# Performance work log

Measured on AMD Instinct MI355X. Metric: run time of the kernel, lower is better.

Reference implementation:

```python
import jax, jax.numpy as jnp
import numpy as np

N = 100_000      # nodes
E = 1_600_000    # edges (avg degree 16)
IN = 512         # in_feats
HID = 4          # hidden_feats (forced equal to num_heads=4 by the mean(h,2) in forward)
H1 = 4           # heads in layer 1
OUT = 128        # out_feats
NEG_SLOPE = 0.2  # DGL GATConv leaky_relu default


def setup_inputs() -> dict:
    key = jax.random.key(0)
    ks = jax.random.split(key, 12)
    nfeats = jax.random.normal(ks[0], (N, IN), jnp.float32)
    efeats = jax.random.normal(ks[1], (E, 8), jnp.float32)  # unused by the module
    src = jax.random.randint(ks[2], (E,), 0, N, dtype=jnp.int32)
    dst = jax.random.randint(ks[3], (E,), 0, N, dtype=jnp.int32)
    # layer 1 params (in=IN, heads=H1, per-head out=HID)
    fc1_w = jax.random.normal(ks[4], (IN, H1 * HID), jnp.float32) / np.sqrt(IN)
    attn_l1 = jax.random.normal(ks[5], (H1, HID), jnp.float32) / np.sqrt(HID)
    attn_r1 = jax.random.normal(ks[6], (H1, HID), jnp.float32) / np.sqrt(HID)
    bias1 = jnp.zeros((H1 * HID,), jnp.float32)
    # layer 2 params (in=H1=4 after mean over feature dim, heads=1, out=OUT)
    fc2_w = jax.random.normal(ks[7], (HID, 1 * OUT), jnp.float32) / np.sqrt(HID)
    attn_l2 = jax.random.normal(ks[8], (1, OUT), jnp.float32) / np.sqrt(OUT)
    attn_r2 = jax.random.normal(ks[9], (1, OUT), jnp.float32) / np.sqrt(OUT)
    bias2 = jnp.zeros((OUT,), jnp.float32)
    return {"nfeats": nfeats, "efeats": efeats, "src": src, "dst": dst,
            "fc1_w": fc1_w, "attn_l1": attn_l1, "attn_r1": attn_r1, "bias1": bias1,
            "fc2_w": fc2_w, "attn_l2": attn_l2, "attn_r2": attn_r2, "bias2": bias2}


def gat_layer(x, src, dst, fc_w, attn_l, attn_r, bias, heads, d_out):
    # projection: (N, in) -> (N, H, D)
    h = (x @ fc_w).reshape(-1, heads, d_out)
    el = jnp.einsum('nhd,hd->nh', h, attn_l)   # (N, H)
    er = jnp.einsum('nhd,hd->nh', h, attn_r)
    e = jax.nn.leaky_relu(el[src] + er[dst], NEG_SLOPE)  # (E, H)
    # segment softmax over incoming edges of each dst node
    m = jax.lax.stop_gradient(jax.ops.segment_max(e, dst, num_segments=N))
    ex = jnp.exp(e - m[dst])
    denom = jax.ops.segment_sum(ex, dst, num_segments=N)
    alpha = ex / denom[dst]                    # (E, H)
    msg = alpha[:, :, None] * h[src]           # (E, H, D)
    rst = jax.ops.segment_sum(msg, dst, num_segments=N)  # (N, H, D)
    return rst + bias.reshape(1, heads, d_out)


def reference(nfeats, efeats, src, dst, fc1_w, attn_l1, attn_r1, bias1,
              fc2_w, attn_l2, attn_r2, bias2):
    h = gat_layer(nfeats, src, dst, fc1_w, attn_l1, attn_r1, bias1, H1, HID)  # (N,4,4)
    h = jnp.mean(h, axis=2)        # faithful to th.mean(h, 2): mean over per-head feat dim -> (N,4)
    h = jax.nn.relu(h)
    h = gat_layer(h, src, dst, fc2_w, attn_l2, attn_r2, bias2, 1, OUT)        # (N,1,OUT)
    return h.reshape(N, OUT)       # flatten(1)
```

## Files before the change

kernel.cpp:

```cpp
#include <hip/hip_runtime.h>
#include <math.h>

#define IN_F 512
#define OUTF 128
#define NEG_SLOPE 0.2f

#define P1T 256
#define TK 16
#define PITCH 20

#define NPB 128
#define NBMAX 784
#define EPB 4096
#define SRCMASK 0x1FFFF
#define CAP 2944

#define WSH_BYTES (IN_F * 12 * 4)
#define XS_BYTES  (P1T * PITCH * 4)
#define SMEM_A    (WSH_BYTES + XS_BYTES)

__global__ void k_prep(const float* __restrict__ fc1, const float* __restrict__ al1,
                       const float* __restrict__ ar1, const float* __restrict__ fc2,
                       const float* __restrict__ al2, const float* __restrict__ ar2,
                       float* __restrict__ wfold, float* __restrict__ w2al,
                       float* __restrict__ w2ar, int* __restrict__ bucketCursor) {
  int t = threadIdx.x;
  if (blockIdx.x == 0) {
    int k = t;
#pragma unroll
    for (int h = 0; h < 4; ++h) {
      float wl = 0.f, wr = 0.f, wb = 0.f;
#pragma unroll
      for (int j = 0; j < 4; ++j) {
        float wv = fc1[k * 16 + h * 4 + j];
        wl = fmaf(wv, al1[h * 4 + j], wl);
        wr = fmaf(wv, ar1[h * 4 + j], wr);
        wb += wv;
      }
      wfold[k * 12 + h] = wl;
      wfold[k * 12 + 4 + h] = wr;
      wfold[k * 12 + 8 + h] = 0.25f * wb;
    }
  } else {
    if (t < 8) {
      int h = t >> 1;
      const float* a = (t & 1) ? ar2 : al2;
      float s = 0.f;
#pragma unroll 16
      for (int c = 0; c < OUTF; ++c) s += fc2[h * OUTF + c] * a[c];
      if (t & 1) w2ar[h] = s; else w2al[h] = s;
    }
    for (int i = t; i < NBMAX; i += 512) bucketCursor[i] = 0;
  }
}

__global__ __launch_bounds__(P1T) void k_A(
    const float* __restrict__ x, const float* __restrict__ wf,
    float* __restrict__ pk1, float* __restrict__ er1, int n,
    const int* __restrict__ src, const int* __restrict__ dst,
    int* __restrict__ bucketCursor, unsigned* __restrict__ ep, int e,
    int projBlocks)
{
  __shared__ __align__(16) char smem[SMEM_A];
  const int t = threadIdx.x;

  if ((int)blockIdx.x < projBlocks) {
    float* wsh = (float*)smem;
    float* xs  = (float*)(smem + WSH_BYTES);
    const int lane = t & 63;
    const int wv = t >> 6;
    const int rowBase = blockIdx.x * P1T;
    const int wrow = rowBase + wv * 64;
    const int myRow = rowBase + t;

    for (int i = t * 4; i < IN_F * 12; i += P1T * 4)
      *(float4*)&wsh[i] = *(const float4*)&wf[i];
    __syncthreads();

    float acc[12];
#pragma unroll
    for (int c = 0; c < 12; ++c) acc[c] = 0.f;

    float4 st[4];
#pragma unroll
    for (int i = 0; i < 4; ++i) {
      int f4 = lane + i * 64;
      int r = f4 >> 2, c4 = (f4 & 3) << 2;
      int row = wrow + r;
      st[i] = (row < n) ? *(const float4*)&x[(size_t)row * IN_F + c4]
                        : make_float4(0.f, 0.f, 0.f, 0.f);
    }

    for (int tile = 0; tile < IN_F / TK; ++tile) {
#pragma unroll
      for (int i = 0; i < 4; ++i) {
        int f4 = lane + i * 64;
        int r = f4 >> 2, c4 = (f4 & 3) << 2;
        *(float4*)&xs[(wv * 64 + r) * PITCH + c4] = st[i];
      }
      if (tile + 1 < IN_F / TK) {
        int k0 = (tile + 1) * TK;
#pragma unroll
        for (int i = 0; i < 4; ++i) {
          int f4 = lane + i * 64;
          int r = f4 >> 2, c4 = (f4 & 3) << 2;
          int row = wrow + r;
          st[i] = (row < n) ? *(const float4*)&x[(size_t)row * IN_F + k0 + c4]
                            : make_float4(0.f, 0.f, 0.f, 0.f);
        }
      }
      asm volatile("s_waitcnt lgkmcnt(0)" ::: "memory");
      __builtin_amdgcn_sched_barrier(0);
      const int kb = tile * TK;
#pragma unroll
      for (int k4 = 0; k4 < 4; ++k4) {
        float4 xv = *(const float4*)&xs[t * PITCH + k4 * 4];
        float xj[4] = {xv.x, xv.y, xv.z, xv.w};
#pragma unroll
        for (int j = 0; j < 4; ++j) {
          const float* wk = &wsh[(kb + k4 * 4 + j) * 12];
          float4 w0 = *(const float4*)&wk[0];
          float4 w1 = *(const float4*)&wk[4];
          float4 w2 = *(const float4*)&wk[8];
          acc[0]  = fmaf(xj[j], w0.x, acc[0]);   acc[1]  = fmaf(xj[j], w0.y, acc[1]);
          acc[2]  = fmaf(xj[j], w0.z, acc[2]);   acc[3]  = fmaf(xj[j], w0.w, acc[3]);
          acc[4]  = fmaf(xj[j], w1.x, acc[4]);   acc[5]  = fmaf(xj[j], w1.y, acc[5]);
          acc[6]  = fmaf(xj[j], w1.z, acc[6]);   acc[7]  = fmaf(xj[j], w1.w, acc[7]);
          acc[8]  = fmaf(xj[j], w2.x, acc[8]);   acc[9]  = fmaf(xj[j], w2.y, acc[9]);
          acc[10] = fmaf(xj[j], w2.z, acc[10]);  acc[11] = fmaf(xj[j], w2.w, acc[11]);
        }
      }
    }

    if (myRow < n) {
      *(float4*)&pk1[(size_t)myRow * 8 + 0] = make_float4(acc[0], acc[1], acc[2], acc[3]);
      *(float4*)&pk1[(size_t)myRow * 8 + 4] = make_float4(acc[8], acc[9], acc[10], acc[11]);
      *(float4*)&er1[(size_t)myRow * 4] = make_float4(acc[4], acc[5], acc[6], acc[7]);
    }
  } else {
    int* hist = (int*)smem;
    int* base = hist + NBMAX;
    int* lcur = base + NBMAX;
    const int bb = blockIdx.x - projBlocks;
    for (int i = t; i < NBMAX; i += P1T) hist[i] = 0;
    __syncthreads();
    int blockBase = bb * EPB;
#pragma unroll
    for (int i = 0; i < EPB / P1T; ++i) {
      int idx = blockBase + t + i * P1T;
      if (idx < e) atomicAdd(&hist[dst[idx] >> 7], 1);
    }
    __syncthreads();
    for (int i = t; i < NBMAX; i += P1T) {
      if (hist[i] > 0) base[i] = atomicAdd(&bucketCursor[i], hist[i]);
      lcur[i] = 0;
    }
    __syncthreads();
#pragma unroll
    for (int i = 0; i < EPB / P1T; ++i) {
      int idx = blockBase + t + i * P1T;
      if (idx < e) {
        int d = dst[idx];
        int b = d >> 7;
        int off = base[b] + atomicAdd(&lcur[b], 1);
        if (off < CAP)
          ep[(size_t)b * CAP + off] = (unsigned)src[idx] | ((unsigned)(d & (NPB - 1)) << 17);
      }
    }
  }
}

__global__ __launch_bounds__(256) void k_B(
    const unsigned* __restrict__ ep, const int* __restrict__ bucketCursor,
    unsigned* __restrict__ ep2, int* __restrict__ nodeBeg, int* __restrict__ nodeEnd,
    const float* __restrict__ pk1, const float* __restrict__ er1,
    const float* __restrict__ bias1,
    const float* __restrict__ w2al, const float* __restrict__ w2ar,
    float* __restrict__ pk2, float* __restrict__ er2, int n)
{
  __shared__ int cnt[NPB];
  __shared__ int scn[NPB];
  __shared__ int cur[NPB];
  __shared__ unsigned lbuf[CAP];
  int t = threadIdx.x;
  int b = blockIdx.x;
  int nodeBase = b * NPB;
  int m = bucketCursor[b];
  if (m > CAP) m = CAP;
  const unsigned* __restrict__ in = ep + (size_t)b * CAP;
  if (t < NPB) cnt[t] = 0;
  __syncthreads();
  for (int j = t; j < m; j += 256) atomicAdd(&cnt[in[j] >> 17], 1);
  __syncthreads();
  if (t < NPB) scn[t] = cnt[t];
  __syncthreads();
  for (int off = 1; off < NPB; off <<= 1) {
    int v = (t < NPB && t >= off) ? scn[t - off] : 0;
    __syncthreads();
    if (t < NPB) scn[t] += v;
    __syncthreads();
  }
  if (t < NPB) {
    int excl = scn[t] - cnt[t];
    int node = nodeBase + t;
    if (node < n) {
      nodeBeg[node] = b * CAP + excl;
      nodeEnd[node] = b * CAP + excl + cnt[t];
    }
    cur[t] = excl;
  }
  __syncthreads();
  for (int j = t; j < m; j += 256) {
    unsigned p = in[j];
    int pos = atomicAdd(&cur[p >> 17], 1);
    lbuf[pos] = p & SRCMASK;
  }
  __syncthreads();
  for (int i = t; i < m; i += 256) ep2[(size_t)b * CAP + i] = lbuf[i];

#pragma unroll
  for (int half = 0; half < 2; ++half) {
    int w = t + half * 256;
    int i = w >> 2, h = w & 3;
    int node = nodeBase + i;
    bool active = node < n;
    float v = 0.f;
    if (active) {
      int beg = scn[i] - cnt[i], end = scn[i];
      float ern = er1[(size_t)node * 4 + h];
      float den = 0.f, num = 0.f;
      for (int j = beg; j < end; ++j) {
        int s = (int)lbuf[j];
        float el = pk1[(size_t)s * 8 + h];
        float hb = pk1[(size_t)s * 8 + 4 + h];
        float eh = el + ern;
        eh = (eh > 0.f) ? eh : NEG_SLOPE * eh;
        float wg = __expf(eh);
        den += wg;
        num = fmaf(wg, hb, num);
      }
      float mb = 0.25f * (bias1[h*4] + bias1[h*4+1] + bias1[h*4+2] + bias1[h*4+3]);
      v = (end > beg) ? num / den : 0.f;
      v += mb;
      v = (v > 0.f) ? v : 0.f;
    }
    float pl = v * w2al[h];
    float pr = v * w2ar[h];
    pl += __shfl_xor(pl, 1); pl += __shfl_xor(pl, 2);
    pr += __shfl_xor(pr, 1); pr += __shfl_xor(pr, 2);
    if (active) {
      pk2[(size_t)node * 8 + h] = v;
      if (h == 0) { pk2[(size_t)node * 8 + 4] = pl; er2[node] = pr; }
    }
  }
}

__global__ __launch_bounds__(256) void k_bagg2(
    const unsigned* __restrict__ ep2, const int* __restrict__ nodeBeg,
    const int* __restrict__ nodeEnd,
    const float* __restrict__ pk2, const float* __restrict__ er2,
    const float* __restrict__ w2, const float* __restrict__ bias2,
    float* __restrict__ out, int n)
{
  __shared__ float gacc[256 * 4];
  __shared__ float w2s[4 * OUTF];
  __shared__ float b2s[OUTF];
  int t = threadIdx.x;
  int nodeBase = blockIdx.x * 256;
  int nn = nodeBase + t;
  for (int i = t; i < 4 * OUTF; i += 256) w2s[i] = w2[i];
  if (t < OUTF) b2s[t] = bias2[t];
  float g0 = 0.f, g1 = 0.f, g2 = 0.f, g3 = 0.f;
  if (nn < n) {
    int beg = nodeBeg[nn], end = nodeEnd[nn];
    float ern = er2[nn];
    float den = 0.f;
    for (int j = beg; j < end; ++j) {
      int s = (int)ep2[j];
      const float* __restrict__ ps = &pk2[(size_t)s * 8];
      float4 hv = *(const float4*)ps;
      float e = ps[4] + ern;
      e = (e > 0.f) ? e : NEG_SLOPE * e;
      float w = __expf(e);
      den += w;
      g0 = fmaf(w, hv.x, g0); g1 = fmaf(w, hv.y, g1);
      g2 = fmaf(w, hv.z, g2); g3 = fmaf(w, hv.w, g3);
    }
    float inv = (end > beg) ? 1.0f / den : 0.f;
    g0 *= inv; g1 *= inv; g2 *= inv; g3 *= inv;
  }
  gacc[t * 4 + 0] = g0; gacc[t * 4 + 1] = g1;
  gacc[t * 4 + 2] = g2; gacc[t * 4 + 3] = g3;
  __syncthreads();
  for (int idx = t; idx < 256 * (OUTF / 2); idx += 256) {
    int i = idx >> 6;
    int node = nodeBase + i;
    if (node >= n) continue;
    int c = (idx & 63) * 2;
    float gx = gacc[i*4], gy = gacc[i*4+1], gz = gacc[i*4+2], gw = gacc[i*4+3];
    float2 o;
    o.x = gx*w2s[c]   + gy*w2s[OUTF+c]   + gz*w2s[2*OUTF+c]   + gw*w2s[3*OUTF+c]   + b2s[c];
    o.y = gx*w2s[c+1] + gy*w2s[OUTF+c+1] + gz*w2s[2*OUTF+c+1] + gw*w2s[3*OUTF+c+1] + b2s[c+1];
    *(float2*)&out[(size_t)node * OUTF + c] = o;
  }
}

extern "C" void kernel_launch(void* const* d_in, const int* in_sizes, int n_in,
                              void* d_out, int out_size, void* d_ws, size_t ws_size,
                              hipStream_t stream) {
  const float* nfeats = (const float*)d_in[0];
  const int*   srcp   = (const int*)d_in[2];
  const int*   dstp   = (const int*)d_in[3];
  const float* fc1    = (const float*)d_in[4];
  const float* al1    = (const float*)d_in[5];
  const float* ar1    = (const float*)d_in[6];
  const float* bias1  = (const float*)d_in[7];
  const float* fc2    = (const float*)d_in[8];
  const float* al2    = (const float*)d_in[9];
  const float* ar2    = (const float*)d_in[10];
  const float* bias2  = (const float*)d_in[11];

  const int N = in_sizes[0] / IN_F;
  const int E = in_sizes[2];
  const int NB = (N + NPB - 1) / NPB;

  float* ws   = (float*)d_ws;
  float* pk1  = ws;
  float* er1  = pk1 + (size_t)8 * N;
  float* pk2  = er1 + (size_t)4 * N;
  float* er2  = pk2 + (size_t)8 * N;
  float* wfold= er2 + N;
  float* w2al = wfold + 512 * 12;
  float* w2ar = w2al + 4;
  int* bucketCursor = (int*)(w2ar + 4);
  int* nodeBeg      = bucketCursor + NBMAX;
  int* nodeEnd      = nodeBeg + N;
  unsigned* ep      = (unsigned*)(nodeEnd + N);
  unsigned* ep2     = ep + (size_t)NB * CAP;

  const int binBlocks = (E + EPB - 1) / EPB;
  const int projBlocks = (N + P1T - 1) / P1T;

  k_prep<<<2, 512, 0, stream>>>(fc1, al1, ar1, fc2, al2, ar2,
                                wfold, w2al, w2ar, bucketCursor);
  k_A<<<projBlocks + binBlocks, P1T, 0, stream>>>(nfeats, wfold, pk1, er1, N,
                                                  srcp, dstp, bucketCursor, ep, E,
                                                  projBlocks);
  k_B<<<NB, 256, 0, stream>>>(ep, bucketCursor, ep2, nodeBeg, nodeEnd,
                              pk1, er1, bias1, w2al, w2ar, pk2, er2, N);
  k_bagg2<<<(N + 255) / 256, 256, 0, stream>>>(ep2, nodeBeg, nodeEnd, pk2, er2,
                                               fc2, bias2, (float*)d_out, N);
}
```

Measured before the change: 151.6 us.

## Use bf16 MFMA with hi/lo split weights for layer-1 projection

```diff
diff --git a/kernel.cpp b/kernel.cpp
--- a/kernel.cpp
+++ b/kernel.cpp
@@ -5,9 +5,13 @@
 #define OUTF 128
 #define NEG_SLOPE 0.2f
 
+typedef __attribute__((ext_vector_type(8))) short bf16x8;
+typedef __attribute__((ext_vector_type(4))) float f32x4;
+
 #define P1T 256
-#define TK 16
-#define PITCH 20
+#define XP 136
+#define NKS 16
+#define BPSH 8192
 
 #define NPB 128
 #define NBMAX 784
@@ -15,15 +19,23 @@
 #define SRCMASK 0x1FFFF
 #define CAP 2944
 
-#define WSH_BYTES (IN_F * 12 * 4)
-#define XS_BYTES  (P1T * PITCH * 4)
-#define SMEM_A    (WSH_BYTES + XS_BYTES)
+#define BP_BYTES (2 * BPSH * 2)
+#define XS_BYTES (4 * 16 * XP * 2)
+#define SMEM_A   (BP_BYTES + XS_BYTES)
+
+__device__ __forceinline__ unsigned pkbf(float a, float b) {
+  unsigned ua = __float_as_uint(a); ua += 0x7FFF + ((ua >> 16) & 1);
+  unsigned ub = __float_as_uint(b); ub += 0x7FFF + ((ub >> 16) & 1);
+  return (ua >> 16) | (ub & 0xFFFF0000u);
+}
 
 __global__ void k_prep(const float* __restrict__ fc1, const float* __restrict__ al1,
                        const float* __restrict__ ar1, const float* __restrict__ fc2,
                        const float* __restrict__ al2, const float* __restrict__ ar2,
-                       float* __restrict__ wfold, float* __restrict__ w2al,
-                       float* __restrict__ w2ar, int* __restrict__ bucketCursor) {
+                       unsigned short* __restrict__ BpHi, unsigned short* __restrict__ BpLo,
+                       float* __restrict__ w2al, float* __restrict__ w2ar,
+                       int* __restrict__ bucketCursor) {
+  __shared__ float wlds[IN_F * 12];
   int t = threadIdx.x;
   if (blockIdx.x == 0) {
     int k = t;
@@ -37,9 +49,33 @@
         wr = fmaf(wv, ar1[h * 4 + j], wr);
         wb += wv;
       }
-      wfold[k * 12 + h] = wl;
-      wfold[k * 12 + 4 + h] = wr;
-      wfold[k * 12 + 8 + h] = 0.25f * wb;
+      wlds[k * 12 + h] = wl;
+      wlds[k * 12 + 4 + h] = wr;
+      wlds[k * 12 + 8 + h] = 0.25f * wb;
+    }
+    __syncthreads();
+    for (int item = t; item < NKS * 64; item += 512) {
+      int s = item >> 6, l = item & 63;
+      int col = l & 15;
+      int kb = s * 32 + ((l >> 4) * 8);
+      unsigned hi[4], lo[4];
+#pragma unroll
+      for (int p = 0; p < 4; ++p) {
+        float w0 = 0.f, w1 = 0.f;
+        if (col < 12) {
+          w0 = wlds[(kb + 2 * p) * 12 + col];
+          w1 = wlds[(kb + 2 * p + 1) * 12 + col];
+        }
+        unsigned u0 = __float_as_uint(w0); u0 += 0x7FFF + ((u0 >> 16) & 1);
+        unsigned u1 = __float_as_uint(w1); u1 += 0x7FFF + ((u1 >> 16) & 1);
+        unsigned h0 = u0 >> 16, h1 = u1 >> 16;
+        hi[p] = h0 | (h1 << 16);
+        float r0 = w0 - __uint_as_float(h0 << 16);
+        float r1 = w1 - __uint_as_float(h1 << 16);
+        lo[p] = pkbf(r0, r1);
+      }
+      *(uint4*)&BpHi[item * 8] = make_uint4(hi[0], hi[1], hi[2], hi[3]);
+      *(uint4*)&BpLo[item * 8] = make_uint4(lo[0], lo[1], lo[2], lo[3]);
     }
   } else {
     if (t < 8) {
@@ -55,7 +91,8 @@
 }
 
 __global__ __launch_bounds__(P1T) void k_A(
-    const float* __restrict__ x, const float* __restrict__ wf,
+    const float* __restrict__ x,
+    const unsigned short* __restrict__ BpHi, const unsigned short* __restrict__ BpLo,
     float* __restrict__ pk1, float* __restrict__ er1, int n,
     const int* __restrict__ src, const int* __restrict__ dst,
     int* __restrict__ bucketCursor, unsigned* __restrict__ ep, int e,
@@ -65,77 +102,76 @@
   const int t = threadIdx.x;
 
   if ((int)blockIdx.x < projBlocks) {
-    float* wsh = (float*)smem;
-    float* xs  = (float*)(smem + WSH_BYTES);
     const int lane = t & 63;
     const int wv = t >> 6;
-    const int rowBase = blockIdx.x * P1T;
-    const int wrow = rowBase + wv * 64;
-    const int myRow = rowBase + t;
-
-    for (int i = t * 4; i < IN_F * 12; i += P1T * 4)
-      *(float4*)&wsh[i] = *(const float4*)&wf[i];
-    __syncthreads();
-
-    float acc[12];
-#pragma unroll
-    for (int c = 0; c < 12; ++c) acc[c] = 0.f;
-
-    float4 st[4];
-#pragma unroll
-    for (int i = 0; i < 4; ++i) {
-      int f4 = lane + i * 64;
-      int r = f4 >> 2, c4 = (f4 & 3) << 2;
-      int row = wrow + r;
-      st[i] = (row < n) ? *(const float4*)&x[(size_t)row * IN_F + c4]
-                        : make_float4(0.f, 0.f, 0.f, 0.f);
-    }
-
-    for (int tile = 0; tile < IN_F / TK; ++tile) {
+    const bf16x8* Bfrag = (const bf16x8*)smem;
+    short* xsw = (short*)(smem + BP_BYTES) + wv * (16 * XP);
+
+    for (int i = t; i < 2 * NKS * 64; i += P1T) {
+      ((uint4*)smem)[i] = (i < NKS * 64) ? ((const uint4*)BpHi)[i]
+                                         : ((const uint4*)BpLo)[i - NKS * 64];
+    }
+    __syncthreads();
+
+    const int totalWaves = projBlocks * 4;
+    const int rtMax = (n + 15) >> 4;
+    for (int rt = blockIdx.x * 4 + wv; rt < rtMax; rt += totalWaves) {
+      const int wrow = rt * 16;
+      const float* __restrict__ xr = x + (size_t)wrow * IN_F;
+      f32x4 acc = {0.f, 0.f, 0.f, 0.f};
+
+      float4 st[8];
+#pragma unroll
+      for (int i = 0; i < 8; ++i) {
+        int f = lane + i * 64;
+        int r = f >> 5, c4 = (f & 31) * 4;
+        st[i] = (wrow + r < n) ? *(const float4*)&xr[(size_t)r * IN_F + c4]
+                               : make_float4(0.f, 0.f, 0.f, 0.f);
+      }
+
+      for (int kt = 0; kt < 4; ++kt) {
+#pragma unroll
+        for (int i = 0; i < 8; ++i) {
+          int f = lane + i * 64;
+          int r = f >> 5, c4 = (f & 31) * 4;
+          uint2 pv; pv.x = pkbf(st[i].x, st[i].y); pv.y = pkbf(st[i].z, st[i].w);
+          *(uint2*)&xsw[r * XP + c4] = pv;
+        }
+        if (kt < 3) {
+          int kb = (kt + 1) * 128;
+#pragma unroll
+          for (int i = 0; i < 8; ++i) {
+            int f = lane + i * 64;
+            int r = f >> 5, c4 = (f & 31) * 4;
+            st[i] = (wrow + r < n) ? *(const float4*)&xr[(size_t)r * IN_F + kb + c4]
+                                   : make_float4(0.f, 0.f, 0.f, 0.f);
+          }
+        }
+        asm volatile("s_waitcnt lgkmcnt(0)" ::: "memory");
+        __builtin_amdgcn_sched_barrier(0);
+#pragma unroll
+        for (int ks = 0; ks < 4; ++ks) {
+          bf16x8 a = *(const bf16x8*)&xsw[(lane & 15) * XP + ks * 32 + ((lane >> 4) * 8)];
+          int bidx = (kt * 4 + ks) * 64 + lane;
+          bf16x8 bh = Bfrag[bidx];
+          bf16x8 bl = Bfrag[NKS * 64 + bidx];
+          acc = __builtin_amdgcn_mfma_f32_16x16x32_bf16(a, bh, acc, 0, 0, 0);
+          acc = __builtin_amdgcn_mfma_f32_16x16x32_bf16(a, bl, acc, 0, 0, 0);
+        }
+      }
+
+      int col = lane & 15;
+      int rbase = wrow + ((lane >> 4) * 4);
 #pragma unroll
       for (int i = 0; i < 4; ++i) {
-        int f4 = lane + i * 64;
-        int r = f4 >> 2, c4 = (f4 & 3) << 2;
-        *(float4*)&xs[(wv * 64 + r) * PITCH + c4] = st[i];
-      }
-      if (tile + 1 < IN_F / TK) {
-        int k0 = (tile + 1) * TK;
-#pragma unroll
-        for (int i = 0; i < 4; ++i) {
-          int f4 = lane + i * 64;
-          int r = f4 >> 2, c4 = (f4 & 3) << 2;
-          int row = wrow + r;
-          st[i] = (row < n) ? *(const float4*)&x[(size_t)row * IN_F + k0 + c4]
-                            : make_float4(0.f, 0.f, 0.f, 0.f);
-        }
-      }
-      asm volatile("s_waitcnt lgkmcnt(0)" ::: "memory");
-      __builtin_amdgcn_sched_barrier(0);
-      const int kb = tile * TK;
-#pragma unroll
-      for (int k4 = 0; k4 < 4; ++k4) {
-        float4 xv = *(const float4*)&xs[t * PITCH + k4 * 4];
-        float xj[4] = {xv.x, xv.y, xv.z, xv.w};
-#pragma unroll
-        for (int j = 0; j < 4; ++j) {
-          const float* wk = &wsh[(kb + k4 * 4 + j) * 12];
-          float4 w0 = *(const float4*)&wk[0];
-          float4 w1 = *(const float4*)&wk[4];
-          float4 w2 = *(const float4*)&wk[8];
-          acc[0]  = fmaf(xj[j], w0.x, acc[0]);   acc[1]  = fmaf(xj[j], w0.y, acc[1]);
-          acc[2]  = fmaf(xj[j], w0.z, acc[2]);   acc[3]  = fmaf(xj[j], w0.w, acc[3]);
-          acc[4]  = fmaf(xj[j], w1.x, acc[4]);   acc[5]  = fmaf(xj[j], w1.y, acc[5]);
-          acc[6]  = fmaf(xj[j], w1.z, acc[6]);   acc[7]  = fmaf(xj[j], w1.w, acc[7]);
-          acc[8]  = fmaf(xj[j], w2.x, acc[8]);   acc[9]  = fmaf(xj[j], w2.y, acc[9]);
-          acc[10] = fmaf(xj[j], w2.z, acc[10]);  acc[11] = fmaf(xj[j], w2.w, acc[11]);
-        }
-      }
-    }
-
-    if (myRow < n) {
-      *(float4*)&pk1[(size_t)myRow * 8 + 0] = make_float4(acc[0], acc[1], acc[2], acc[3]);
-      *(float4*)&pk1[(size_t)myRow * 8 + 4] = make_float4(acc[8], acc[9], acc[10], acc[11]);
-      *(float4*)&er1[(size_t)myRow * 4] = make_float4(acc[4], acc[5], acc[6], acc[7]);
+        int row = rbase + i;
+        if (row < n) {
+          float v = acc[i];
+          if (col < 4)       pk1[(size_t)row * 8 + col] = v;
+          else if (col < 8)  er1[(size_t)row * 4 + (col - 4)] = v;
+          else if (col < 12) pk1[(size_t)row * 8 + 4 + (col - 8)] = v;
+        }
+      }
     }
   } else {
     int* hist = (int*)smem;
@@ -329,21 +365,22 @@
   float* er1  = pk1 + (size_t)8 * N;
   float* pk2  = er1 + (size_t)4 * N;
   float* er2  = pk2 + (size_t)8 * N;
-  float* wfold= er2 + N;
-  float* w2al = wfold + 512 * 12;
+  float* w2al = er2 + N;
   float* w2ar = w2al + 4;
-  int* bucketCursor = (int*)(w2ar + 4);
+  unsigned short* BpHi = (unsigned short*)(w2ar + 4);
+  unsigned short* BpLo = BpHi + BPSH;
+  int* bucketCursor = (int*)(BpLo + BPSH);
   int* nodeBeg      = bucketCursor + NBMAX;
   int* nodeEnd      = nodeBeg + N;
   unsigned* ep      = (unsigned*)(nodeEnd + N);
   unsigned* ep2     = ep + (size_t)NB * CAP;
 
   const int binBlocks = (E + EPB - 1) / EPB;
-  const int projBlocks = (N + P1T - 1) / P1T;
+  const int projBlocks = 391;
 
   k_prep<<<2, 512, 0, stream>>>(fc1, al1, ar1, fc2, al2, ar2,
-                                wfold, w2al, w2ar, bucketCursor);
-  k_A<<<projBlocks + binBlocks, P1T, 0, stream>>>(nfeats, wfold, pk1, er1, N,
+                                BpHi, BpLo, w2al, w2ar, bucketCursor);
+  k_A<<<projBlocks + binBlocks, P1T, 0, stream>>>(nfeats, BpHi, BpLo, pk1, er1, N,
                                                   srcp, dstp, bucketCursor, ep, E,
                                                   projBlocks);
   k_B<<<NB, 256, 0, stream>>>(ep, bucketCursor, ep2, nodeBeg, nodeEnd,
```

After: 135.3 us. 1.12x faster.
